# Kernel optimization log

Hardware: AMD Instinct MI355X
Metric: run time of the kernel (lower is better)

The kernel has to match this reference:

```python
import jax, jax.numpy as jnp
import numpy as np

NUM_HEADS = 8


def setup_inputs() -> dict:
    key = jax.random.key(0)
    k1, k2, k3 = jax.random.split(key, 3)
    B, N, C = 4, 2048, 256
    x = jax.random.normal(k1, (B, N, C), dtype=jnp.float32)
    qkv_w = jax.random.normal(k2, (3 * C, C), dtype=jnp.float32) * (C ** -0.5)
    proj_w = jax.random.normal(k3, (C, C), dtype=jnp.float32) * (C ** -0.5)
    proj_b = jnp.zeros((C,), dtype=jnp.float32)
    return {"x": x, "qkv_w": qkv_w, "proj_w": proj_w, "proj_b": proj_b}


def reference(x, qkv_w, proj_w, proj_b):
    B, N, C = x.shape
    H = NUM_HEADS
    hd = C // H
    scale = hd ** -0.5
    # 1x1 conv over [B,C,N,1] == per-token linear: [B,3C,N]
    qkv = jnp.einsum('bnc,dc->bdn', x, qkv_w)
    # faithful to torch reshape+chunk: per-head interleaved q/k/v layout
    qkv = qkv.reshape(B, H, 3 * hd, N)
    q, k, v = jnp.split(qkv, 3, axis=2)  # each [B,H,hd,N]
    # attn[b,h,i,j] = sum_d k[b,h,d,i] * q[b,h,d,j], scaled
    attn = jnp.einsum('bhdi,bhdj->bhij', k, q) * scale  # [B,H,Nk,Nq]
    attn = jax.nn.softmax(attn, axis=-2)  # softmax over key axis (dim=-2)
    out = jnp.einsum('bhdi,bhij->bhdj', v, attn)  # [B,H,hd,N]
    out = out.reshape(B, C, N, 1)
    # proj 1x1 conv with bias
    out = jnp.einsum('bcnq,dc->bdnq', out, proj_w) + proj_b[None, :, None, None]
    return out
```

## Files before the change

kernel.cpp:

```cpp
#include <hip/hip_runtime.h>
#include <hip/hip_bf16.h>

#define NTOK 2048
#define CDIM 256
#define HEADS 8
#define HD 32
#define SCALE 0.17677669529663687f

typedef __attribute__((ext_vector_type(8))) short short8;
typedef __attribute__((ext_vector_type(4))) float float4v;
typedef unsigned short ushort_t;
typedef unsigned int uint_t;

#define MFMA(a, b, c) __builtin_amdgcn_mfma_f32_16x16x32_bf16(a, b, c, 0, 0, 0)

__device__ __forceinline__ uint_t cvt_pk(float lo, float hi) {
    uint_t r;
    asm("v_cvt_pk_bf16_f32 %0, %1, %2" : "=v"(r) : "v"(lo), "v"(hi));
    return r;
}
__device__ __forceinline__ ushort_t f2bf(float f) {
    union { __hip_bfloat16 h; ushort_t u; } cv;
    cv.h = __float2bfloat16(f);
    return cv.u;
}

__global__ __launch_bounds__(256) void cvt_bf16(const float* __restrict__ in,
                                                uint4* __restrict__ out, int n8) {
    int i = blockIdx.x * 256 + threadIdx.x;
    if (i >= n8) return;
    const float4* p = (const float4*)in + (size_t)2 * i;
    float4 a = p[0], bq = p[1];
    uint4 r;
    r.x = cvt_pk(a.x, a.y);  r.y = cvt_pk(a.z, a.w);
    r.z = cvt_pk(bq.x, bq.y); r.w = cvt_pk(bq.z, bq.w);
    out[i] = r;
}

__global__ __launch_bounds__(256) void qkv_mfma(const ushort_t* __restrict__ x_bf,
                                                const ushort_t* __restrict__ w_bf,
                                                ushort_t* __restrict__ q_t,
                                                ushort_t* __restrict__ k_t,
                                                ushort_t* __restrict__ v_) {
    const int tid = threadIdx.x, wave = tid >> 6, lane = tid & 63;
    const int l15 = lane & 15, g = lane >> 4;
    const int b = blockIdx.z;
    const int dtile = blockIdx.x * 128 + (wave >> 1) * 64;
    const int ntile = blockIdx.y * 128 + (wave & 1) * 64;

    const ushort_t* A = w_bf + (size_t)dtile * CDIM + g * 8;
    const ushort_t* B = x_bf + ((size_t)b * NTOK + ntile) * CDIM + g * 8;

    float4v acc[4][4];
    #pragma unroll
    for (int i = 0; i < 4; ++i)
        #pragma unroll
        for (int j = 0; j < 4; ++j)
            #pragma unroll
            for (int r = 0; r < 4; ++r) acc[i][j][r] = 0.f;

    #pragma unroll
    for (int k0 = 0; k0 < CDIM; k0 += 32) {
        short8 af[4], bf[4];
        #pragma unroll
        for (int i = 0; i < 4; ++i)
            af[i] = *(const short8*)&A[(size_t)(l15 + 16 * i) * CDIM + k0];
        #pragma unroll
        for (int j = 0; j < 4; ++j)
            bf[j] = *(const short8*)&B[(size_t)(l15 + 16 * j) * CDIM + k0];
        #pragma unroll
        for (int i = 0; i < 4; ++i)
            #pragma unroll
            for (int j = 0; j < 4; ++j)
                acc[i][j] = MFMA(af[i], bf[j], acc[i][j]);
    }

    #pragma unroll
    for (int i = 0; i < 4; ++i) {
        #pragma unroll
        for (int r = 0; r < 4; ++r) {
            const int d = dtile + i * 16 + g * 4 + r;
            const int h = (d * 683) >> 16;
            const int t = d - h * 96;
            const size_t bh = (size_t)(b * HEADS + h);
            #pragma unroll
            for (int j = 0; j < 4; ++j) {
                const int n = ntile + j * 16 + l15;
                const float val = acc[i][j][r];
                if (t < 64) {
                    const int sel = t >> 5, dm = t & 31;
                    ushort_t* dst = (sel ? k_t : q_t) + bh * ((size_t)NTOK * HD)
                                    + (size_t)n * HD + dm;
                    *dst = f2bf(sel ? val : val * SCALE);
                } else {
                    v_[bh * ((size_t)NTOK * HD) + (size_t)(t - 64) * NTOK + n] = f2bf(val);
                }
            }
        }
    }
}

__global__ __launch_bounds__(256) void attn_mfma(const ushort_t* __restrict__ q_t,
                                                 const ushort_t* __restrict__ k_t,
                                                 const ushort_t* __restrict__ v_,
                                                 ushort_t* __restrict__ preT) {
    __shared__ uint_t pt[4][2][16 * 20];
    const int tid = threadIdx.x, wave = tid >> 6, lane = tid & 63;
    const int l15 = lane & 15, g = lane >> 4;
    const int bh = blockIdx.y, b = bh >> 3, h = bh & 7;
    const int j0 = blockIdx.x * 128 + wave * 32;

    const ushort_t* qb = q_t + (size_t)bh * (NTOK * HD);
    const ushort_t* kb = k_t + (size_t)bh * (NTOK * HD);
    const ushort_t* vb = v_  + (size_t)bh * (NTOK * HD);

    short8 qf0 = *(const short8*)&qb[(size_t)(j0 + l15) * HD + g * 8];
    short8 qf1 = *(const short8*)&qb[(size_t)(j0 + 16 + l15) * HD + g * 8];

    const float4v z4 = {0.f, 0.f, 0.f, 0.f};
    float4v o00 = z4, o01 = z4, o10 = z4, o11 = z4;
    float lsum0 = 0.f, lsum1 = 0.f;

    uint_t* pt0 = &pt[wave][0][0];
    uint_t* pt1 = &pt[wave][1][0];
    const int wbase = l15 * 20 + g * 2;
    const int rbase = l15 * 20 + g * 4;

    for (int i0 = 0; i0 < NTOK; i0 += 32) {
        short8 aK0 = *(const short8*)&kb[(size_t)(i0 + l15) * HD + g * 8];
        short8 aK1 = *(const short8*)&kb[(size_t)(i0 + 16 + l15) * HD + g * 8];

        float4v s00 = MFMA(aK0, qf0, z4);
        float4v s10 = MFMA(aK1, qf0, z4);
        float4v s01 = MFMA(aK0, qf1, z4);
        float4v s11 = MFMA(aK1, qf1, z4);

        {
            float e0[4], e1[4];
            #pragma unroll
            for (int r = 0; r < 4; ++r) { e0[r] = __expf(s00[r]); e1[r] = __expf(s10[r]); }
            lsum0 += e0[0]+e0[1]+e0[2]+e0[3] + e1[0]+e1[1]+e1[2]+e1[3];
            pt0[wbase]     = cvt_pk(e0[0], e0[1]);
            pt0[wbase + 1] = cvt_pk(e0[2], e0[3]);
            pt0[wbase + 8] = cvt_pk(e1[0], e1[1]);
            pt0[wbase + 9] = cvt_pk(e1[2], e1[3]);
        }
        {
            float e0[4], e1[4];
            #pragma unroll
            for (int r = 0; r < 4; ++r) { e0[r] = __expf(s01[r]); e1[r] = __expf(s11[r]); }
            lsum1 += e0[0]+e0[1]+e0[2]+e0[3] + e1[0]+e1[1]+e1[2]+e1[3];
            pt1[wbase]     = cvt_pk(e0[0], e0[1]);
            pt1[wbase + 1] = cvt_pk(e0[2], e0[3]);
            pt1[wbase + 8] = cvt_pk(e1[0], e1[1]);
            pt1[wbase + 9] = cvt_pk(e1[2], e1[3]);
        }

        short8 pB0 = *(const short8*)&pt0[rbase];
        short8 pB1 = *(const short8*)&pt1[rbase];

        short8 aV0 = *(const short8*)&vb[(size_t)l15 * NTOK + i0 + g * 8];
        short8 aV1 = *(const short8*)&vb[(size_t)(16 + l15) * NTOK + i0 + g * 8];

        o00 = MFMA(aV0, pB0, o00);
        o01 = MFMA(aV0, pB1, o01);
        o10 = MFMA(aV1, pB0, o10);
        o11 = MFMA(aV1, pB1, o11);
    }

    lsum0 += __shfl_xor(lsum0, 16, 64); lsum0 += __shfl_xor(lsum0, 32, 64);
    lsum1 += __shfl_xor(lsum1, 16, 64); lsum1 += __shfl_xor(lsum1, 32, 64);
    const float rl0 = 1.f / lsum0, rl1 = 1.f / lsum1;

    ushort_t* pb_ = preT + ((size_t)b * NTOK + j0) * CDIM + h * HD;
    #pragma unroll
    for (int r = 0; r < 4; ++r) {
        const int d0 = g * 4 + r, d1 = 16 + g * 4 + r;
        pb_[(size_t)l15 * CDIM + d0]        = f2bf(o00[r] * rl0);
        pb_[(size_t)(16 + l15) * CDIM + d0] = f2bf(o01[r] * rl1);
        pb_[(size_t)l15 * CDIM + d1]        = f2bf(o10[r] * rl0);
        pb_[(size_t)(16 + l15) * CDIM + d1] = f2bf(o11[r] * rl1);
    }
}

__global__ __launch_bounds__(256) void proj_mfma(const ushort_t* __restrict__ preT,
                                                 const ushort_t* __restrict__ w2_bf,
                                                 const float* __restrict__ pb,
                                                 float* __restrict__ out) {
    const int tid = threadIdx.x, wave = tid >> 6, lane = tid & 63;
    const int l15 = lane & 15, g = lane >> 4;
    const int b = blockIdx.z;
    const int dtile = blockIdx.x * 128 + (wave >> 1) * 64;
    const int ntile = blockIdx.y * 128 + (wave & 1) * 64;

    const ushort_t* A = w2_bf + (size_t)dtile * CDIM + g * 8;
    const ushort_t* B = preT + ((size_t)b * NTOK + ntile) * CDIM + g * 8;

    float4v acc[4][4];
    #pragma unroll
    for (int i = 0; i < 4; ++i)
        #pragma unroll
        for (int j = 0; j < 4; ++j)
            #pragma unroll
            for (int r = 0; r < 4; ++r) acc[i][j][r] = 0.f;

    #pragma unroll
    for (int k0 = 0; k0 < CDIM; k0 += 32) {
        short8 af[4], bf[4];
        #pragma unroll
        for (int i = 0; i < 4; ++i)
            af[i] = *(const short8*)&A[(size_t)(l15 + 16 * i) * CDIM + k0];
        #pragma unroll
        for (int j = 0; j < 4; ++j)
            bf[j] = *(const short8*)&B[(size_t)(l15 + 16 * j) * CDIM + k0];
        #pragma unroll
        for (int i = 0; i < 4; ++i)
            #pragma unroll
            for (int j = 0; j < 4; ++j)
                acc[i][j] = MFMA(af[i], bf[j], acc[i][j]);
    }

    #pragma unroll
    for (int i = 0; i < 4; ++i) {
        #pragma unroll
        for (int r = 0; r < 4; ++r) {
            const int d = dtile + i * 16 + g * 4 + r;
            const float bias = pb[d];
            float* orow = out + ((size_t)b * CDIM + d) * NTOK + ntile;
            #pragma unroll
            for (int j = 0; j < 4; ++j)
                orow[j * 16 + l15] = acc[i][j][r] + bias;
        }
    }
}

extern "C" void kernel_launch(void* const* d_in, const int* in_sizes, int n_in,
                              void* d_out, int out_size, void* d_ws, size_t ws_size,
                              hipStream_t stream) {
    const float* x      = (const float*)d_in[0];
    const float* qkv_w  = (const float*)d_in[1];
    const float* proj_w = (const float*)d_in[2];
    const float* proj_b = (const float*)d_in[3];
    float* out = (float*)d_out;

    char* ws = (char*)d_ws;
    ushort_t* x_bf  = (ushort_t*)(ws);
    ushort_t* preT  = (ushort_t*)(ws);
    ushort_t* w_bf  = (ushort_t*)(ws + (size_t)4 * 1024 * 1024);
    ushort_t* w2_bf = (ushort_t*)(ws + (size_t)4608 * 1024);
    ushort_t* q_t   = (ushort_t*)(ws + (size_t)5 * 1024 * 1024);
    ushort_t* k_t   = (ushort_t*)(ws + (size_t)9 * 1024 * 1024);
    ushort_t* v_    = (ushort_t*)(ws + (size_t)13 * 1024 * 1024);

    cvt_bf16<<<1024, 256, 0, stream>>>(x,      (uint4*)x_bf,  262144);
    cvt_bf16<<<96,   256, 0, stream>>>(qkv_w,  (uint4*)w_bf,  24576);
    cvt_bf16<<<32,   256, 0, stream>>>(proj_w, (uint4*)w2_bf, 8192);
    qkv_mfma<<<dim3(6, 16, 4), 256, 0, stream>>>(x_bf, w_bf, q_t, k_t, v_);
    attn_mfma<<<dim3(NTOK / 128, 4 * HEADS), 256, 0, stream>>>(q_t, k_t, v_, preT);
    proj_mfma<<<dim3(2, 16, 4), 256, 0, stream>>>(preT, w2_bf, proj_b, out);
}
```

Before: 153.5 us.

## Split attention key range across wave pairs and shrink GEMM tiles for occupancy

The attention kernel now splits each query tile's key loop across two waves. Their partial outputs and row sums are merged through shared memory before normalizing, which doubles the number of blocks and shortens each wave's serial loop. The QKV and projection GEMMs use smaller per-wave tiles to launch more blocks. The QKV epilogue now picks q, k or v once per 32-row tile and writes packed bf16 pairs, and the attention output uses packed stores. This costs an extra shared-memory buffer, a block barrier, and less register-level reuse in the GEMMs.

```diff
diff --git a/kernel.cpp b/kernel.cpp
--- a/kernel.cpp
+++ b/kernel.cpp
@@ -45,15 +45,15 @@
     const int tid = threadIdx.x, wave = tid >> 6, lane = tid & 63;
     const int l15 = lane & 15, g = lane >> 4;
     const int b = blockIdx.z;
-    const int dtile = blockIdx.x * 128 + (wave >> 1) * 64;
+    const int dtile = blockIdx.x * 64 + (wave >> 1) * 32;
     const int ntile = blockIdx.y * 128 + (wave & 1) * 64;
 
     const ushort_t* A = w_bf + (size_t)dtile * CDIM + g * 8;
     const ushort_t* B = x_bf + ((size_t)b * NTOK + ntile) * CDIM + g * 8;
 
-    float4v acc[4][4];
-    #pragma unroll
-    for (int i = 0; i < 4; ++i)
+    float4v acc[2][4];
+    #pragma unroll
+    for (int i = 0; i < 2; ++i)
         #pragma unroll
         for (int j = 0; j < 4; ++j)
             #pragma unroll
@@ -61,42 +61,45 @@
 
     #pragma unroll
     for (int k0 = 0; k0 < CDIM; k0 += 32) {
-        short8 af[4], bf[4];
-        #pragma unroll
-        for (int i = 0; i < 4; ++i)
+        short8 af[2], bf[4];
+        #pragma unroll
+        for (int i = 0; i < 2; ++i)
             af[i] = *(const short8*)&A[(size_t)(l15 + 16 * i) * CDIM + k0];
         #pragma unroll
         for (int j = 0; j < 4; ++j)
             bf[j] = *(const short8*)&B[(size_t)(l15 + 16 * j) * CDIM + k0];
         #pragma unroll
-        for (int i = 0; i < 4; ++i)
+        for (int i = 0; i < 2; ++i)
             #pragma unroll
             for (int j = 0; j < 4; ++j)
                 acc[i][j] = MFMA(af[i], bf[j], acc[i][j]);
     }
 
-    #pragma unroll
-    for (int i = 0; i < 4; ++i) {
-        #pragma unroll
-        for (int r = 0; r < 4; ++r) {
-            const int d = dtile + i * 16 + g * 4 + r;
-            const int h = (d * 683) >> 16;
-            const int t = d - h * 96;
-            const size_t bh = (size_t)(b * HEADS + h);
+    const int hq = (dtile * 683) >> 16;
+    const int tl = dtile - hq * 96;
+    const size_t bh = (size_t)(b * HEADS + hq);
+
+    if (tl == 64) {
+        #pragma unroll
+        for (int i = 0; i < 2; ++i)
+            #pragma unroll
+            for (int j = 0; j < 4; ++j)
+                #pragma unroll
+                for (int r = 0; r < 4; ++r)
+                    v_[bh * ((size_t)NTOK * HD) + (size_t)(i * 16 + g * 4 + r) * NTOK
+                       + ntile + j * 16 + l15] = f2bf(acc[i][j][r]);
+    } else {
+        ushort_t* base = (tl ? k_t : q_t) + bh * ((size_t)NTOK * HD);
+        const float mul = tl ? 1.f : SCALE;
+        #pragma unroll
+        for (int i = 0; i < 2; ++i)
             #pragma unroll
             for (int j = 0; j < 4; ++j) {
-                const int n = ntile + j * 16 + l15;
-                const float val = acc[i][j][r];
-                if (t < 64) {
-                    const int sel = t >> 5, dm = t & 31;
-                    ushort_t* dst = (sel ? k_t : q_t) + bh * ((size_t)NTOK * HD)
-                                    + (size_t)n * HD + dm;
-                    *dst = f2bf(sel ? val : val * SCALE);
-                } else {
-                    v_[bh * ((size_t)NTOK * HD) + (size_t)(t - 64) * NTOK + n] = f2bf(val);
-                }
+                uint2 pk;
+                pk.x = cvt_pk(acc[i][j][0] * mul, acc[i][j][1] * mul);
+                pk.y = cvt_pk(acc[i][j][2] * mul, acc[i][j][3] * mul);
+                *(uint2*)&base[(size_t)(ntile + j * 16 + l15) * HD + i * 16 + g * 4] = pk;
             }
-        }
     }
 }
 
@@ -105,10 +108,12 @@
                                                  const ushort_t* __restrict__ v_,
                                                  ushort_t* __restrict__ preT) {
     __shared__ uint_t pt[4][2][16 * 20];
+    __shared__ float comb[4][64][18];
     const int tid = threadIdx.x, wave = tid >> 6, lane = tid & 63;
     const int l15 = lane & 15, g = lane >> 4;
-    const int bh = blockIdx.y, b = bh >> 3, h = bh & 7;
-    const int j0 = blockIdx.x * 128 + wave * 32;
+    const int bh = blockIdx.x, b = bh >> 3, h = bh & 7;
+    const int j0 = blockIdx.y * 64 + (wave >> 1) * 32;
+    const int khalf = wave & 1;
 
     const ushort_t* qb = q_t + (size_t)bh * (NTOK * HD);
     const ushort_t* kb = k_t + (size_t)bh * (NTOK * HD);
@@ -126,7 +131,8 @@
     const int wbase = l15 * 20 + g * 2;
     const int rbase = l15 * 20 + g * 4;
 
-    for (int i0 = 0; i0 < NTOK; i0 += 32) {
+    const int kbeg = khalf * 1024, kend = kbeg + 1024;
+    for (int i0 = kbeg; i0 < kend; i0 += 32) {
         short8 aK0 = *(const short8*)&kb[(size_t)(i0 + l15) * HD + g * 8];
         short8 aK1 = *(const short8*)&kb[(size_t)(i0 + 16 + l15) * HD + g * 8];
 
@@ -170,16 +176,34 @@
 
     lsum0 += __shfl_xor(lsum0, 16, 64); lsum0 += __shfl_xor(lsum0, 32, 64);
     lsum1 += __shfl_xor(lsum1, 16, 64); lsum1 += __shfl_xor(lsum1, 32, 64);
-    const float rl0 = 1.f / lsum0, rl1 = 1.f / lsum1;
-
-    ushort_t* pb_ = preT + ((size_t)b * NTOK + j0) * CDIM + h * HD;
+
+    float* cb = &comb[wave][lane][0];
     #pragma unroll
     for (int r = 0; r < 4; ++r) {
-        const int d0 = g * 4 + r, d1 = 16 + g * 4 + r;
-        pb_[(size_t)l15 * CDIM + d0]        = f2bf(o00[r] * rl0);
-        pb_[(size_t)(16 + l15) * CDIM + d0] = f2bf(o01[r] * rl1);
-        pb_[(size_t)l15 * CDIM + d1]        = f2bf(o10[r] * rl0);
-        pb_[(size_t)(16 + l15) * CDIM + d1] = f2bf(o11[r] * rl1);
+        cb[r] = o00[r]; cb[4 + r] = o01[r]; cb[8 + r] = o10[r]; cb[12 + r] = o11[r];
+    }
+    cb[16] = lsum0; cb[17] = lsum1;
+    __syncthreads();
+
+    if (khalf == 0) {
+        const float* cp = &comb[wave ^ 1][lane][0];
+        #pragma unroll
+        for (int r = 0; r < 4; ++r) {
+            o00[r] += cp[r]; o01[r] += cp[4 + r]; o10[r] += cp[8 + r]; o11[r] += cp[12 + r];
+        }
+        const float rl0 = 1.f / (lsum0 + cp[16]);
+        const float rl1 = 1.f / (lsum1 + cp[17]);
+
+        ushort_t* pb_ = preT + ((size_t)b * NTOK + j0) * CDIM + h * HD;
+        uint2 w0, w1, w2, w3;
+        w0.x = cvt_pk(o00[0] * rl0, o00[1] * rl0); w0.y = cvt_pk(o00[2] * rl0, o00[3] * rl0);
+        w1.x = cvt_pk(o01[0] * rl1, o01[1] * rl1); w1.y = cvt_pk(o01[2] * rl1, o01[3] * rl1);
+        w2.x = cvt_pk(o10[0] * rl0, o10[1] * rl0); w2.y = cvt_pk(o10[2] * rl0, o10[3] * rl0);
+        w3.x = cvt_pk(o11[0] * rl1, o11[1] * rl1); w3.y = cvt_pk(o11[2] * rl1, o11[3] * rl1);
+        *(uint2*)&pb_[(size_t)l15 * CDIM + g * 4] = w0;
+        *(uint2*)&pb_[(size_t)(16 + l15) * CDIM + g * 4] = w1;
+        *(uint2*)&pb_[(size_t)l15 * CDIM + 16 + g * 4] = w2;
+        *(uint2*)&pb_[(size_t)(16 + l15) * CDIM + 16 + g * 4] = w3;
     }
 }
 
@@ -190,45 +214,45 @@
     const int tid = threadIdx.x, wave = tid >> 6, lane = tid & 63;
     const int l15 = lane & 15, g = lane >> 4;
     const int b = blockIdx.z;
-    const int dtile = blockIdx.x * 128 + (wave >> 1) * 64;
-    const int ntile = blockIdx.y * 128 + (wave & 1) * 64;
+    const int dtile = blockIdx.x * 64 + (wave >> 1) * 32;
+    const int ntile = blockIdx.y * 64 + (wave & 1) * 32;
 
     const ushort_t* A = w2_bf + (size_t)dtile * CDIM + g * 8;
     const ushort_t* B = preT + ((size_t)b * NTOK + ntile) * CDIM + g * 8;
 
-    float4v acc[4][4];
-    #pragma unroll
-    for (int i = 0; i < 4; ++i)
-        #pragma unroll
-        for (int j = 0; j < 4; ++j)
+    float4v acc[2][2];
+    #pragma unroll
+    for (int i = 0; i < 2; ++i)
+        #pragma unroll
+        for (int j = 0; j < 2; ++j)
             #pragma unroll
             for (int r = 0; r < 4; ++r) acc[i][j][r] = 0.f;
 
     #pragma unroll
     for (int k0 = 0; k0 < CDIM; k0 += 32) {
-        short8 af[4], bf[4];
-        #pragma unroll
-        for (int i = 0; i < 4; ++i)
+        short8 af[2], bf[2];
+        #pragma unroll
+        for (int i = 0; i < 2; ++i)
             af[i] = *(const short8*)&A[(size_t)(l15 + 16 * i) * CDIM + k0];
         #pragma unroll
-        for (int j = 0; j < 4; ++j)
+        for (int j = 0; j < 2; ++j)
             bf[j] = *(const short8*)&B[(size_t)(l15 + 16 * j) * CDIM + k0];
         #pragma unroll
-        for (int i = 0; i < 4; ++i)
-            #pragma unroll
-            for (int j = 0; j < 4; ++j)
+        for (int i = 0; i < 2; ++i)
+            #pragma unroll
+            for (int j = 0; j < 2; ++j)
                 acc[i][j] = MFMA(af[i], bf[j], acc[i][j]);
     }
 
     #pragma unroll
-    for (int i = 0; i < 4; ++i) {
+    for (int i = 0; i < 2; ++i) {
         #pragma unroll
         for (int r = 0; r < 4; ++r) {
             const int d = dtile + i * 16 + g * 4 + r;
             const float bias = pb[d];
             float* orow = out + ((size_t)b * CDIM + d) * NTOK + ntile;
             #pragma unroll
-            for (int j = 0; j < 4; ++j)
+            for (int j = 0; j < 2; ++j)
                 orow[j * 16 + l15] = acc[i][j][r] + bias;
         }
     }
@@ -255,7 +279,7 @@
     cvt_bf16<<<1024, 256, 0, stream>>>(x,      (uint4*)x_bf,  262144);
     cvt_bf16<<<96,   256, 0, stream>>>(qkv_w,  (uint4*)w_bf,  24576);
     cvt_bf16<<<32,   256, 0, stream>>>(proj_w, (uint4*)w2_bf, 8192);
-    qkv_mfma<<<dim3(6, 16, 4), 256, 0, stream>>>(x_bf, w_bf, q_t, k_t, v_);
-    attn_mfma<<<dim3(NTOK / 128, 4 * HEADS), 256, 0, stream>>>(q_t, k_t, v_, preT);
-    proj_mfma<<<dim3(2, 16, 4), 256, 0, stream>>>(preT, w2_bf, proj_b, out);
-}
+    qkv_mfma<<<dim3(12, 16, 4), 256, 0, stream>>>(x_bf, w_bf, q_t, k_t, v_);
+    attn_mfma<<<dim3(4 * HEADS, NTOK / 64), 256, 0, stream>>>(q_t, k_t, v_, preT);
+    proj_mfma<<<dim3(4, 32, 4), 256, 0, stream>>>(preT, w2_bf, proj_b, out);
+}
```

Measured after the change: 148.6 us. 1.03x faster.
